# Optimization experiments

Measured on AMD Instinct MI355X. Metric: run time of the kernel, lower is better.

The kernel has to match this reference:

```python
import jax, jax.numpy as jnp
import numpy as np

D_MODEL = 1024
NHEAD = 16
NUM_KV = 4
D_K = D_MODEL // NHEAD          # 64
GROUP = NHEAD // NUM_KV          # 4 query heads per kv head
ROPE_BASE = 10000.0


def _rope(x, seq_len):
    """Apply rotary embedding. x: [B, h, S, d_k], positions 0..seq_len-1."""
    half = D_K // 2
    inv_freq = 1.0 / (ROPE_BASE ** (jnp.arange(0, D_K, 2, dtype=jnp.float32) / D_K))
    t = jnp.arange(seq_len, dtype=jnp.float32)
    freqs = jnp.outer(t, inv_freq)                      # [S, d_k/2]
    emb = jnp.concatenate([freqs, freqs], axis=-1)      # [S, d_k]
    cos, sin = jnp.cos(emb), jnp.sin(emb)               # broadcast over B, h
    x1, x2 = x[..., :half], x[..., half:]
    rot = jnp.concatenate([-x2, x1], axis=-1)
    return x * cos + rot * sin


def setup_inputs() -> dict:
    key = jax.random.key(0)
    ks = jax.random.split(key, 12)
    B, S = 2, 2048
    s_in = 1.0 / np.sqrt(D_MODEL)
    inp = {
        "query": jax.random.normal(ks[0], (B, S, D_MODEL), jnp.float32),
        "key":   jax.random.normal(ks[1], (B, S, D_MODEL), jnp.float32),
        "value": jax.random.normal(ks[2], (B, S, D_MODEL), jnp.float32),
        "Wq": jax.random.normal(ks[3], (D_MODEL, D_MODEL), jnp.float32) * s_in,
        "bq": jnp.zeros((D_MODEL,), jnp.float32),
        "Wk": jax.random.normal(ks[4], (NUM_KV * D_K, D_MODEL), jnp.float32) * s_in,
        "bk": jnp.zeros((NUM_KV * D_K,), jnp.float32),
        "Wv": jax.random.normal(ks[5], (NUM_KV * D_K, D_MODEL), jnp.float32) * s_in,
        "bv": jnp.zeros((NUM_KV * D_K,), jnp.float32),
        "Wo": jax.random.normal(ks[6], (D_MODEL, D_MODEL), jnp.float32) * s_in,
        "bo": jnp.zeros((D_MODEL,), jnp.float32),
    }
    return inp


def reference(query, key, value, Wq, bq, Wk, bk, Wv, bv, Wo, bo):
    B, S, _ = query.shape
    T = key.shape[1]
    # projections (torch Linear: x @ W^T + b)
    Q = (query @ Wq.T + bq).reshape(B, S, NHEAD, D_K).transpose(0, 2, 1, 3)   # [B,H,S,dk]
    K = (key   @ Wk.T + bk).reshape(B, T, NUM_KV, D_K).transpose(0, 2, 1, 3)  # [B,KV,T,dk]
    V = (value @ Wv.T + bv).reshape(B, T, NUM_KV, D_K).transpose(0, 2, 1, 3)
    # fused RoPE (start_pos = 0)
    Q = _rope(Q, S)
    K = _rope(K, T)
    # expand kv heads (repeat_interleave on head dim)
    Kr = jnp.repeat(K, GROUP, axis=1)   # [B,H,T,dk]
    Vr = jnp.repeat(V, GROUP, axis=1)
    scale = 1.0 / np.sqrt(D_K)
    scores = jnp.einsum("bhsd,bhtd->bhst", Q, Kr) * scale   # [B,H,S,T]
    attn = jax.nn.softmax(scores, axis=-1)                    # dropout = eval/no-op
    context = jnp.einsum("bhst,bhtd->bhsd", attn, Vr)        # [B,H,S,dk]
    context = context.transpose(0, 2, 1, 3).reshape(B, S, D_MODEL)
    return context @ Wo.T + bo
```

## Files before the change

### kernel.cpp

```cpp
#include <hip/hip_runtime.h>
#include <hip/hip_bf16.h>

typedef __hip_bfloat16 bf16;
typedef __attribute__((ext_vector_type(8))) short short8;
typedef __attribute__((ext_vector_type(4))) short short4v;
typedef __attribute__((ext_vector_type(4))) float f32x4;
typedef __attribute__((ext_vector_type(4))) float float4v;

static __device__ inline short f2bf(float f){
  __hip_bfloat16 h = __float2bfloat16(f);
  return *reinterpret_cast<short*>(&h);
}

static __device__ __forceinline__ unsigned cvt_pk_bf16(float lo, float hi){
  unsigned r;
  asm("v_cvt_pk_bf16_f32 %0, %1, %2" : "=v"(r) : "v"(lo), "v"(hi));
  return r;
}

static __device__ __forceinline__ float exp2_fast(float x){
  float r;
  asm("v_exp_f32 %0, %1" : "=v"(r) : "v"(x));
  return r;
}

static __device__ __forceinline__ float max3f(float a, float b, float c){
  float r;
  asm("v_max3_f32 %0, %1, %2, %3" : "=v"(r) : "v"(a), "v"(b), "v"(c));
  return r;
}

static __device__ inline short8 load8(const float* p){
  float4v a = *reinterpret_cast<const float4v*>(p);
  float4v b = *reinterpret_cast<const float4v*>(p + 4);
  short8 r;
  unsigned* u = reinterpret_cast<unsigned*>(&r);
  u[0] = cvt_pk_bf16(a[0], a[1]);
  u[1] = cvt_pk_bf16(a[2], a[3]);
  u[2] = cvt_pk_bf16(b[0], b[1]);
  u[3] = cvt_pk_bf16(b[2], b[3]);
  return r;
}
static __device__ inline short8 load8(const bf16* p){
  return *reinterpret_cast<const short8*>(p);
}

typedef __attribute__((address_space(1))) const unsigned int gas_u32;
typedef __attribute__((address_space(3))) unsigned int las_u32;
static __device__ __forceinline__ void gload16(const void* g, void* l){
  __builtin_amdgcn_global_load_lds((gas_u32*)g, (las_u32*)l, 16, 0, 0);
}

template<int N>
static __device__ __forceinline__ void vm_barrier(){
  if constexpr (N == 8) asm volatile("s_waitcnt vmcnt(8)" ::: "memory");
  else if constexpr (N == 4) asm volatile("s_waitcnt vmcnt(4)" ::: "memory");
  else if constexpr (N == 2) asm volatile("s_waitcnt vmcnt(2)" ::: "memory");
  else asm volatile("s_waitcnt vmcnt(0)" ::: "memory");
  __builtin_amdgcn_s_barrier();
  __builtin_amdgcn_sched_barrier(0);
}

#define CVT_Q   0
#define CVT_K   4194304
#define CVT_V   8388608
#define CVT_WQ  12582912
#define CVT_WK  13631488
#define CVT_WV  13893632
#define CVT_WO  14155776
#define CVT_TOT 15204352
__global__ void cvt_kernel(bf16* __restrict__ dst, float* __restrict__ tab,
    const float* q, const float* k, const float* v,
    const float* wq, const float* wk, const float* wv, const float* wo){
  if (blockIdx.x < 256){
    const int idx = blockIdx.x * 256 + threadIdx.x;
    const int d = idx & 31, s = idx >> 5;
    const float ang = (float)s * exp2f(-0.41524101186092030f * (float)d);
    float sn, cs;
    sincosf(ang, &sn, &cs);
    tab[idx*2] = cs; tab[idx*2+1] = sn;
  }
  const size_t i8 = ((size_t)blockIdx.x * 256 + threadIdx.x) * 8;
  const float* src; size_t off;
  if      (i8 < CVT_K ){ src = q;  off = i8; }
  else if (i8 < CVT_V ){ src = k;  off = i8 - CVT_K; }
  else if (i8 < CVT_WQ){ src = v;  off = i8 - CVT_V; }
  else if (i8 < CVT_WK){ src = wq; off = i8 - CVT_WQ; }
  else if (i8 < CVT_WV){ src = wk; off = i8 - CVT_WK; }
  else if (i8 < CVT_WO){ src = wv; off = i8 - CVT_WV; }
  else                 { src = wo; off = i8 - CVT_WO; }
  *reinterpret_cast<short8*>(reinterpret_cast<short*>(dst) + i8) = load8(src + off);
}

template<int MODE>
__device__ __forceinline__ void gemm_bt_v2(
    short* lds, void* __restrict__ Cout,
    const bf16* __restrict__ A, const bf16* __restrict__ B,
    const float* __restrict__ bias, const float* __restrict__ tab,
    int ntile, int N, int K)
{
  const int NK = K >> 5;
  const int n0 = ntile * 128, m0 = blockIdx.y * 128;
  const int tid = threadIdx.x, w = tid >> 6, lane = tid & 63;
  const int wm = w >> 1, wn = w & 1, lr = lane & 15, lg = lane >> 4;
  const int r0 = w*32 + (lane >> 2), r1 = r0 + 16;
  const int c0 = ((lane & 3) ^ ((r0 >> 1) & 3)) * 8;
  const int c1 = ((lane & 3) ^ ((r1 >> 1) & 3)) * 8;
  const bf16* A0 = A + (size_t)(m0 + r0) * K + c0;
  const bf16* A1 = A + (size_t)(m0 + r1) * K + c1;
  const bf16* B0 = B + (size_t)(n0 + r0) * K + c0;
  const bf16* B1 = B + (size_t)(n0 + r1) * K + c1;
  const int ldsW = (w*32) * 32;
  int offA[4], offB[4];
  #pragma unroll
  for (int i = 0; i < 4; i++){
    const int ra = wm*64 + i*16 + lr;
    offA[i] = ra*64 + ((lg ^ ((ra >> 1) & 3)) * 16);
    const int rb = wn*64 + i*16 + lr;
    offB[i] = rb*64 + ((lg ^ ((rb >> 1) & 3)) * 16);
  }
  auto stage = [&](int t){
    short* bufA = lds + (t & 3) * 8192;
    short* bufB = bufA + 4096;
    gload16(A0 + t*32, bufA + ldsW);
    gload16(A1 + t*32, bufA + ldsW + 512);
    gload16(B0 + t*32, bufB + ldsW);
    gload16(B1 + t*32, bufB + ldsW + 512);
  };
  f32x4 acc[4][4] = {};
  stage(0); stage(1);
  for (int t = 0; t < NK; t++){
    if (t + 2 < NK){ stage(t + 2); vm_barrier<8>(); }
    else if (t + 1 < NK){ vm_barrier<4>(); }
    else { vm_barrier<0>(); }
    const char* bufA = (const char*)(lds + (t & 3) * 8192);
    const char* bufB = bufA + 8192;
    short8 af[4], bfm[4];
    #pragma unroll
    for (int mt = 0; mt < 4; mt++) af[mt]  = *(const short8*)(bufA + offA[mt]);
    #pragma unroll
    for (int nt = 0; nt < 4; nt++) bfm[nt] = *(const short8*)(bufB + offB[nt]);
    __builtin_amdgcn_s_setprio(1);
    #pragma unroll
    for (int mt = 0; mt < 4; mt++)
      #pragma unroll
      for (int nt = 0; nt < 4; nt++)
        acc[mt][nt] = __builtin_amdgcn_mfma_f32_16x16x32_bf16(af[mt], bfm[nt], acc[mt][nt], 0, 0, 0);
    __builtin_amdgcn_s_setprio(0);
  }
  if constexpr (MODE == 0){
    float* C = (float*)Cout;
    #pragma unroll
    for (int mt = 0; mt < 4; mt++){
      #pragma unroll
      for (int nt = 0; nt < 4; nt++){
        const int col = n0 + wn*64 + nt*16 + lr;
        const float bv = bias[col];
        const int rbase = m0 + wm*64 + mt*16 + lg*4;
        #pragma unroll
        for (int i = 0; i < 4; i++)
          C[(size_t)(rbase + i) * N + col] = acc[mt][nt][i] + bv;
      }
    }
  } else if constexpr (MODE == 1 || MODE == 2){
    bf16* dst = (bf16*)Cout;
    constexpr int NH = (MODE == 1) ? 16 : 4;
    constexpr float SC = (MODE == 1) ? 0.18033688011112042f : 1.0f;
    #pragma unroll
    for (int mt = 0; mt < 4; mt++){
      #pragma unroll
      for (int nt = 0; nt < 2; nt++){
        const int col = n0 + wn*64 + nt*16 + lr;
        const int d = col & 63;
        const int hh = col >> 6;
        const float b1 = bias[col], b2 = bias[col + 32];
        #pragma unroll
        for (int i = 0; i < 4; i++){
          const int m = m0 + wm*64 + mt*16 + lg*4 + i;
          const int s = m & 2047, bb = m >> 11;
          const float cs = tab[(s*32 + d)*2], sn = tab[(s*32 + d)*2 + 1];
          const float x1 = acc[mt][nt][i] + b1;
          const float x2 = acc[mt][nt+2][i] + b2;
          const size_t o = ((size_t)(bb*NH + hh) * 2048 + s) * 64 + d;
          dst[o]      = __float2bfloat16((x1*cs - x2*sn) * SC);
          dst[o + 32] = __float2bfloat16((x2*cs + x1*sn) * SC);
        }
      }
    }
  } else {
    bf16* dst = (bf16*)Cout;
    #pragma unroll
    for (int mt = 0; mt < 4; mt++){
      #pragma unroll
      for (int nt = 0; nt < 4; nt++){
        const int col = n0 + wn*64 + nt*16 + lr;
        const int kv = col >> 6, d = col & 63;
        const float bv = bias[col];
        #pragma unroll
        for (int i = 0; i < 4; i++){
          const int m = m0 + wm*64 + mt*16 + lg*4 + i;
          const int s = m & 2047, bb = m >> 11;
          dst[((size_t)(bb*4 + kv) * 64 + d) * 2048 + s] = __float2bfloat16(acc[mt][nt][i] + bv);
        }
      }
    }
  }
}

__global__ __launch_bounds__(256, 2) void gemm_qkv_kernel(
    bf16* Qa, bf16* Ka, bf16* Va, const bf16* cvt,
    const float* bq, const float* bk, const float* bv, const float* tab){
  __shared__ short lds[4 * 8192];
  const int x = blockIdx.x;
  if (x < 8)
    gemm_bt_v2<1>(lds, Qa, cvt + CVT_Q, cvt + CVT_WQ, bq, tab, x,    1024, 1024);
  else if (x < 10)
    gemm_bt_v2<2>(lds, Ka, cvt + CVT_K, cvt + CVT_WK, bk, tab, x-8,  256, 1024);
  else
    gemm_bt_v2<3>(lds, Va, cvt + CVT_V, cvt + CVT_WV, bv, tab, x-10, 256, 1024);
}
__global__ __launch_bounds__(256, 2) void gemm_out_kernel(
    float* C, const bf16* ctx, const bf16* cvt, const float* bo){
  __shared__ short lds[4 * 8192];
  gemm_bt_v2<0>(lds, C, ctx, cvt + CVT_WO, bo, nullptr, blockIdx.x, 1024, 1024);
}

__global__ __launch_bounds__(256, 2) void attn_kernel(
    bf16* __restrict__ ctx, const bf16* __restrict__ Qa,
    const bf16* __restrict__ Ka, const bf16* __restrict__ Vt)
{
  __shared__ short Klds[4][64 * 64];
  __shared__ short Vlds[4][64 * 64];
  const int bh = blockIdx.y, b = bh >> 4, h = bh & 15, kvh = h >> 2;
  const int q0 = blockIdx.x * 128;
  const int tid = threadIdx.x, w = tid >> 6, lane = tid & 63;
  const int lr = lane & 15, lg = lane >> 4;
  const bf16* Qbase = Qa + (size_t)bh * 2048 * 64;
  const bf16* Kbase = Ka + (size_t)(b*4 + kvh) * 2048 * 64;
  const bf16* Vbase = Vt + (size_t)(b*4 + kvh) * 64 * 2048;

  short8 qf[2][2];
  #pragma unroll
  for (int qt = 0; qt < 2; qt++){
    qf[qt][0] = load8(Qbase + (size_t)(q0 + w*32 + qt*16 + lr) * 64 + lg*8);
    qf[qt][1] = load8(Qbase + (size_t)(q0 + w*32 + qt*16 + lr) * 64 + 32 + lg*8);
  }

  const int xsw = (lr & 7) << 4;
  const int koff0 = lr*128 + ((lg*16) ^ xsw);
  const int koff1 = lr*128 + ((64 + lg*16) ^ xsw);
  int voff[2][2];
  #pragma unroll
  for (int kkA = 0; kkA < 2; kkA++)
    #pragma unroll
    for (int hh = 0; hh < 2; hh++)
      voff[kkA][hh] = lr*128 + ((kkA*64 + lg*8 + hh*32) ^ xsw);

  const int l8 = lane >> 3;
  const int ch = (lane & 7) ^ l8;
  const bf16* kSrc = Kbase + (size_t)(w*16 + l8) * 64 + ch*8;
  const bf16* vSrc = Vbase + (size_t)(w*16 + l8) * 2048 + ch*8;
  auto stage = [&](int bi, int t){
    short* Kd = &Klds[bi][(w*16) * 64];
    short* Vd = &Vlds[bi][(w*16) * 64];
    const bf16* ks = kSrc + (size_t)t * 64 * 64;
    const bf16* vs = vSrc + t * 64;
    gload16(ks,           Kd);
    gload16(ks + 8*64,    Kd + 8*64);
    gload16(vs,           Vd);
    gload16(vs + 8*2048,  Vd + 8*64);
  };

  float mrow[2] = {-1e30f, -1e30f};
  f32x4 o[2][4] = {};
  f32x4 acc_l[2] = {};
  short8 ones;
  #pragma unroll
  for (int j = 0; j < 4; j++) reinterpret_cast<unsigned*>(&ones)[j] = 0x3F803F80u;

  auto qk = [&](const char* Kc, f32x4 (&st)[4][2]){
    __builtin_amdgcn_s_setprio(1);
    #pragma unroll
    for (int mt = 0; mt < 4; mt++){
      short8 kf0 = *reinterpret_cast<const short8*>(Kc + mt*2048 + koff0);
      short8 kf1 = *reinterpret_cast<const short8*>(Kc + mt*2048 + koff1);
      #pragma unroll
      for (int qt = 0; qt < 2; qt++){
        st[mt][qt] = __builtin_amdgcn_mfma_f32_16x16x32_bf16(kf0, qf[qt][0], (f32x4){0.f,0.f,0.f,0.f}, 0, 0, 0);
        st[mt][qt] = __builtin_amdgcn_mfma_f32_16x16x32_bf16(kf1, qf[qt][1], st[mt][qt], 0, 0, 0);
      }
    }
    __builtin_amdgcn_s_setprio(0);
  };

  auto softmax_pv = [&](f32x4 (&st)[4][2], const char* Vc){
    short8 pf[2][2];
    #pragma unroll
    for (int qt = 0; qt < 2; qt++){
      const float m0 = max3f(st[0][qt][0], st[0][qt][1], st[0][qt][2]);
      const float m1 = max3f(st[0][qt][3], st[1][qt][0], st[1][qt][1]);
      const float m2 = max3f(st[1][qt][2], st[1][qt][3], st[2][qt][0]);
      const float m3 = max3f(st[2][qt][1], st[2][qt][2], st[2][qt][3]);
      const float m4 = max3f(st[3][qt][0], st[3][qt][1], st[3][qt][2]);
      float mx = fmaxf(max3f(m0, m1, m2), max3f(m3, m4, st[3][qt][3]));
      if (__any(mx > mrow[qt] + 8.0f)){
        mx = fmaxf(mx, __shfl_xor(mx, 16));
        mx = fmaxf(mx, __shfl_xor(mx, 32));
        const float nm = fmaxf(mrow[qt], mx);
        const float alpha = exp2_fast(mrow[qt] - nm);
        mrow[qt] = nm;
        float ab[4];
        #pragma unroll
        for (int i = 0; i < 4; i++) ab[i] = __shfl(alpha, lg*4 + i);
        #pragma unroll
        for (int dt = 0; dt < 4; dt++)
          #pragma unroll
          for (int i = 0; i < 4; i++)
            o[qt][dt][i] *= ab[i];
        #pragma unroll
        for (int i = 0; i < 4; i++) acc_l[qt][i] *= ab[i];
      }
      unsigned* pw = reinterpret_cast<unsigned*>(&pf[qt][0]);
      #pragma unroll
      for (int j = 0; j < 8; j++){
        const int mt = j >> 1, i0 = (j & 1) * 2;
        const float e0 = exp2_fast(st[mt][qt][i0]     - mrow[qt]);
        const float e1 = exp2_fast(st[mt][qt][i0 + 1] - mrow[qt]);
        pw[j] = cvt_pk_bf16(e0, e1);
      }
    }
    __builtin_amdgcn_s_setprio(1);
    #pragma unroll
    for (int qt = 0; qt < 2; qt++){
      acc_l[qt] = __builtin_amdgcn_mfma_f32_16x16x32_bf16(pf[qt][0], ones, acc_l[qt], 0, 0, 0);
      acc_l[qt] = __builtin_amdgcn_mfma_f32_16x16x32_bf16(pf[qt][1], ones, acc_l[qt], 0, 0, 0);
    }
    #pragma unroll
    for (int dt = 0; dt < 4; dt++){
      #pragma unroll
      for (int kkA = 0; kkA < 2; kkA++){
        short8 vf;
        *reinterpret_cast<short4v*>(&vf) =
            *reinterpret_cast<const short4v*>(Vc + dt*2048 + voff[kkA][0]);
        *reinterpret_cast<short4v*>(reinterpret_cast<short*>(&vf) + 4) =
            *reinterpret_cast<const short4v*>(Vc + dt*2048 + voff[kkA][1]);
        #pragma unroll
        for (int qt = 0; qt < 2; qt++)
          o[qt][dt] = __builtin_amdgcn_mfma_f32_16x16x32_bf16(pf[qt][kkA], vf, o[qt][dt], 0, 0, 0);
      }
    }
    __builtin_amdgcn_s_setprio(0);
  };

  f32x4 stA[4][2], stB[4][2];

  stage(0, 0); stage(1, 1);
  vm_barrier<4>();
  qk((const char*)&Klds[0][0], stA);

  for (int tt = 0; tt < 32; tt += 2){
    if (tt + 2 < 32){ stage((tt+2) & 3, tt+2); vm_barrier<4>(); }
    else vm_barrier<0>();
    qk((const char*)&Klds[(tt+1) & 3][0], stB);
    softmax_pv(stA, (const char*)&Vlds[tt & 3][0]);
    if (tt + 3 < 32){ stage((tt+3) & 3, tt+3); vm_barrier<4>(); }
    else vm_barrier<0>();
    if (tt + 2 < 32) qk((const char*)&Klds[(tt+2) & 3][0], stA);
    softmax_pv(stB, (const char*)&Vlds[(tt+1) & 3][0]);
  }

  #pragma unroll
  for (int qt = 0; qt < 2; qt++){
    float lb[4];
    #pragma unroll
    for (int i = 0; i < 4; i++) lb[i] = 1.0f / acc_l[qt][i];
    #pragma unroll
    for (int dt = 0; dt < 4; dt++){
      #pragma unroll
      for (int i = 0; i < 4; i++){
        const int q = q0 + w*32 + qt*16 + lg*4 + i;
        ctx[(size_t)(b*2048 + q) * 1024 + h*64 + dt*16 + lr] =
            __float2bfloat16(o[qt][dt][i] * lb[i]);
      }
    }
  }
}

extern "C" void kernel_launch(void* const* d_in, const int* in_sizes, int n_in,
                              void* d_out, int out_size, void* d_ws, size_t ws_size,
                              hipStream_t stream)
{
  const float* query = (const float*)d_in[0];
  const float* key   = (const float*)d_in[1];
  const float* value = (const float*)d_in[2];
  const float* Wq = (const float*)d_in[3];
  const float* bq = (const float*)d_in[4];
  const float* Wk = (const float*)d_in[5];
  const float* bk = (const float*)d_in[6];
  const float* Wv = (const float*)d_in[7];
  const float* bv = (const float*)d_in[8];
  const float* Wo = (const float*)d_in[9];
  const float* bo = (const float*)d_in[10];
  float* out = (float*)d_out;

  char* ws = (char*)d_ws;
  size_t off = 0;
  float* tab = (float*)(ws + off); off += (size_t)2048 * 32 * 2 * 4;
  bf16*  Qa  = (bf16*)(ws + off);  off += (size_t)32 * 2048 * 64 * 2;
  bf16*  Ka  = (bf16*)(ws + off);  off += (size_t)8 * 2048 * 64 * 2;
  bf16*  Va  = (bf16*)(ws + off);  off += (size_t)8 * 64 * 2048 * 2;
  bf16*  ctx = (bf16*)(ws + off);  off += (size_t)2 * 2048 * 1024 * 2;
  bf16*  cvt = (bf16*)(ws + off);  off += (size_t)CVT_TOT * 2;

  cvt_kernel<<<CVT_TOT / 8 / 256, 256, 0, stream>>>(cvt, tab, query, key, value, Wq, Wk, Wv, Wo);
  gemm_qkv_kernel<<<dim3(12, 32), 256, 0, stream>>>(Qa, Ka, Va, cvt, bq, bk, bv, tab);
  attn_kernel<<<dim3(16, 32), 256, 0, stream>>>(ctx, Qa, Ka, Va);
  gemm_out_kernel<<<dim3(8, 32), 256, 0, stream>>>(out, ctx, cvt, bo);
}
```

Baseline: 106.5 us.

## Fuse fp32 activation conversion into QKV GEMM and remap attention block order

The QKV projection GEMM now loads fp32 activations straight into LDS through a three-buffer pipeline and converts them to bf16 in registers before the MFMAs. The conversion kernel therefore only handles the weights. This is meant to remove the large activation round-trip through a bf16 workspace. The attention grid index is also remapped so that concurrently running blocks share KV heads, to improve cache reuse. In exchange, the GEMM loads twice as many bytes per A tile and spends extra ALU on conversions.

```diff
diff --git a/kernel.cpp b/kernel.cpp
--- a/kernel.cpp
+++ b/kernel.cpp
@@ -54,23 +54,19 @@
 template<int N>
 static __device__ __forceinline__ void vm_barrier(){
   if constexpr (N == 8) asm volatile("s_waitcnt vmcnt(8)" ::: "memory");
+  else if constexpr (N == 6) asm volatile("s_waitcnt vmcnt(6)" ::: "memory");
   else if constexpr (N == 4) asm volatile("s_waitcnt vmcnt(4)" ::: "memory");
-  else if constexpr (N == 2) asm volatile("s_waitcnt vmcnt(2)" ::: "memory");
   else asm volatile("s_waitcnt vmcnt(0)" ::: "memory");
   __builtin_amdgcn_s_barrier();
   __builtin_amdgcn_sched_barrier(0);
 }
 
-#define CVT_Q   0
-#define CVT_K   4194304
-#define CVT_V   8388608
-#define CVT_WQ  12582912
-#define CVT_WK  13631488
-#define CVT_WV  13893632
-#define CVT_WO  14155776
-#define CVT_TOT 15204352
+#define CW_WQ  0
+#define CW_WK  1048576
+#define CW_WV  1310720
+#define CW_WO  1572864
+#define CW_TOT 2621440
 __global__ void cvt_kernel(bf16* __restrict__ dst, float* __restrict__ tab,
-    const float* q, const float* k, const float* v,
     const float* wq, const float* wk, const float* wv, const float* wo){
   if (blockIdx.x < 256){
     const int idx = blockIdx.x * 256 + threadIdx.x;
@@ -82,22 +78,144 @@
   }
   const size_t i8 = ((size_t)blockIdx.x * 256 + threadIdx.x) * 8;
   const float* src; size_t off;
-  if      (i8 < CVT_K ){ src = q;  off = i8; }
-  else if (i8 < CVT_V ){ src = k;  off = i8 - CVT_K; }
-  else if (i8 < CVT_WQ){ src = v;  off = i8 - CVT_V; }
-  else if (i8 < CVT_WK){ src = wq; off = i8 - CVT_WQ; }
-  else if (i8 < CVT_WV){ src = wk; off = i8 - CVT_WK; }
-  else if (i8 < CVT_WO){ src = wv; off = i8 - CVT_WV; }
-  else                 { src = wo; off = i8 - CVT_WO; }
+  if      (i8 < CW_WK){ src = wq; off = i8; }
+  else if (i8 < CW_WV){ src = wk; off = i8 - CW_WK; }
+  else if (i8 < CW_WO){ src = wv; off = i8 - CW_WV; }
+  else                { src = wo; off = i8 - CW_WO; }
   *reinterpret_cast<short8*>(reinterpret_cast<short*>(dst) + i8) = load8(src + off);
 }
 
 template<int MODE>
-__device__ __forceinline__ void gemm_bt_v2(
-    short* lds, void* __restrict__ Cout,
-    const bf16* __restrict__ A, const bf16* __restrict__ B,
+__device__ __forceinline__ void gemm_f32a(
+    char* lds, void* __restrict__ Cout,
+    const float* __restrict__ A, const bf16* __restrict__ B,
     const float* __restrict__ bias, const float* __restrict__ tab,
     int ntile, int N, int K)
+{
+  const int NK = K >> 5;
+  const int n0 = ntile * 128, m0 = blockIdx.y * 128;
+  const int tid = threadIdx.x, w = tid >> 6, lane = tid & 63;
+  const int wm = w >> 1, wn = w & 1, lr = lane & 15, lg = lane >> 4;
+  const int l8 = lane >> 3, gA = lane & 7;
+  const float* Asrc[4];
+  #pragma unroll
+  for (int j = 0; j < 4; j++)
+    Asrc[j] = A + (size_t)(m0 + w*32 + j*8 + l8) * K + ((gA ^ l8) * 4);
+  const int s4 = lane >> 2, gB = lane & 3;
+  const bf16* Bsrc[2];
+  #pragma unroll
+  for (int j = 0; j < 2; j++)
+    Bsrc[j] = B + (size_t)(n0 + w*32 + j*16 + s4) * K + ((gB ^ ((s4 >> 1) & 3)) * 8);
+  const int swA = lr & 7, swB = (lr >> 1) & 3;
+  int offAlo[4], offAhi[4], offB[4];
+  #pragma unroll
+  for (int i = 0; i < 4; i++){
+    const int ra = wm*64 + i*16 + lr;
+    offAlo[i] = ra*128 + ((2*lg)     ^ swA) * 16;
+    offAhi[i] = ra*128 + ((2*lg + 1) ^ swA) * 16;
+    const int rb = wn*64 + i*16 + lr;
+    offB[i]   = rb*64  + ((lg ^ swB) * 16);
+  }
+  auto stage = [&](char* buf, int t){
+    char* dA = buf + w*4096;
+    char* dB = buf + 16384 + w*2048;
+    #pragma unroll
+    for (int j = 0; j < 4; j++) gload16(Asrc[j] + t*32, dA + j*1024);
+    #pragma unroll
+    for (int j = 0; j < 2; j++) gload16(Bsrc[j] + t*32, dB + j*1024);
+  };
+  char* b0 = lds;
+  char* b1 = lds + 24576;
+  char* b2 = lds + 49152;
+  f32x4 acc[4][4] = {};
+  stage(b0, 0); stage(b1, 1);
+  for (int t = 0; t < NK; t++){
+    if (t < NK-1) vm_barrier<6>(); else vm_barrier<0>();
+    if (t + 2 < NK) stage(b2, t + 2);
+    short8 af[4], bfm[4];
+    #pragma unroll
+    for (int i = 0; i < 4; i++){
+      float4v lo = *reinterpret_cast<const float4v*>(b0 + offAlo[i]);
+      float4v hi = *reinterpret_cast<const float4v*>(b0 + offAhi[i]);
+      unsigned* u = reinterpret_cast<unsigned*>(&af[i]);
+      u[0] = cvt_pk_bf16(lo[0], lo[1]); u[1] = cvt_pk_bf16(lo[2], lo[3]);
+      u[2] = cvt_pk_bf16(hi[0], hi[1]); u[3] = cvt_pk_bf16(hi[2], hi[3]);
+    }
+    #pragma unroll
+    for (int i = 0; i < 4; i++)
+      bfm[i] = *reinterpret_cast<const short8*>(b0 + 16384 + offB[i]);
+    __builtin_amdgcn_s_setprio(1);
+    #pragma unroll
+    for (int mt = 0; mt < 4; mt++)
+      #pragma unroll
+      for (int nt = 0; nt < 4; nt++)
+        acc[mt][nt] = __builtin_amdgcn_mfma_f32_16x16x32_bf16(af[mt], bfm[nt], acc[mt][nt], 0, 0, 0);
+    __builtin_amdgcn_s_setprio(0);
+    char* tmp = b0; b0 = b1; b1 = b2; b2 = tmp;
+  }
+  if constexpr (MODE == 1 || MODE == 2){
+    bf16* dst = (bf16*)Cout;
+    constexpr int NH = (MODE == 1) ? 16 : 4;
+    constexpr float SC = (MODE == 1) ? 0.18033688011112042f : 1.0f;
+    #pragma unroll
+    for (int mt = 0; mt < 4; mt++){
+      #pragma unroll
+      for (int nt = 0; nt < 2; nt++){
+        const int col = n0 + wn*64 + nt*16 + lr;
+        const int d = col & 63;
+        const int hh = col >> 6;
+        const float b1v = bias[col], b2v = bias[col + 32];
+        #pragma unroll
+        for (int i = 0; i < 4; i++){
+          const int m = m0 + wm*64 + mt*16 + lg*4 + i;
+          const int s = m & 2047, bb = m >> 11;
+          const float cs = tab[(s*32 + d)*2], sn = tab[(s*32 + d)*2 + 1];
+          const float x1 = acc[mt][nt][i] + b1v;
+          const float x2 = acc[mt][nt+2][i] + b2v;
+          const size_t o = ((size_t)(bb*NH + hh) * 2048 + s) * 64 + d;
+          dst[o]      = __float2bfloat16((x1*cs - x2*sn) * SC);
+          dst[o + 32] = __float2bfloat16((x2*cs + x1*sn) * SC);
+        }
+      }
+    }
+  } else {
+    bf16* dst = (bf16*)Cout;
+    #pragma unroll
+    for (int mt = 0; mt < 4; mt++){
+      #pragma unroll
+      for (int nt = 0; nt < 4; nt++){
+        const int col = n0 + wn*64 + nt*16 + lr;
+        const int kv = col >> 6, d = col & 63;
+        const float bv = bias[col];
+        #pragma unroll
+        for (int i = 0; i < 4; i++){
+          const int m = m0 + wm*64 + mt*16 + lg*4 + i;
+          const int s = m & 2047, bb = m >> 11;
+          dst[((size_t)(bb*4 + kv) * 64 + d) * 2048 + s] = __float2bfloat16(acc[mt][nt][i] + bv);
+        }
+      }
+    }
+  }
+}
+
+__global__ __launch_bounds__(256, 2) void gemm_qkv_kernel(
+    bf16* Qa, bf16* Ka, bf16* Va,
+    const float* query, const float* key, const float* value, const bf16* cw,
+    const float* bq, const float* bk, const float* bv, const float* tab){
+  __shared__ char lds[3 * 24576];
+  const int x = blockIdx.x;
+  if (x < 8)
+    gemm_f32a<1>(lds, Qa, query, cw + CW_WQ, bq, tab, x,    1024, 1024);
+  else if (x < 10)
+    gemm_f32a<2>(lds, Ka, key,   cw + CW_WK, bk, tab, x-8,  256, 1024);
+  else
+    gemm_f32a<3>(lds, Va, value, cw + CW_WV, bv, tab, x-10, 256, 1024);
+}
+
+__device__ __forceinline__ void gemm_bt_out(
+    short* lds, float* __restrict__ C,
+    const bf16* __restrict__ A, const bf16* __restrict__ B,
+    const float* __restrict__ bias, int ntile, int N, int K)
 {
   const int NK = K >> 5;
   const int n0 = ntile * 128, m0 = blockIdx.y * 128;
@@ -148,81 +266,24 @@
         acc[mt][nt] = __builtin_amdgcn_mfma_f32_16x16x32_bf16(af[mt], bfm[nt], acc[mt][nt], 0, 0, 0);
     __builtin_amdgcn_s_setprio(0);
   }
-  if constexpr (MODE == 0){
-    float* C = (float*)Cout;
-    #pragma unroll
-    for (int mt = 0; mt < 4; mt++){
-      #pragma unroll
-      for (int nt = 0; nt < 4; nt++){
-        const int col = n0 + wn*64 + nt*16 + lr;
-        const float bv = bias[col];
-        const int rbase = m0 + wm*64 + mt*16 + lg*4;
-        #pragma unroll
-        for (int i = 0; i < 4; i++)
-          C[(size_t)(rbase + i) * N + col] = acc[mt][nt][i] + bv;
-      }
-    }
-  } else if constexpr (MODE == 1 || MODE == 2){
-    bf16* dst = (bf16*)Cout;
-    constexpr int NH = (MODE == 1) ? 16 : 4;
-    constexpr float SC = (MODE == 1) ? 0.18033688011112042f : 1.0f;
-    #pragma unroll
-    for (int mt = 0; mt < 4; mt++){
-      #pragma unroll
-      for (int nt = 0; nt < 2; nt++){
-        const int col = n0 + wn*64 + nt*16 + lr;
-        const int d = col & 63;
-        const int hh = col >> 6;
-        const float b1 = bias[col], b2 = bias[col + 32];
-        #pragma unroll
-        for (int i = 0; i < 4; i++){
-          const int m = m0 + wm*64 + mt*16 + lg*4 + i;
-          const int s = m & 2047, bb = m >> 11;
-          const float cs = tab[(s*32 + d)*2], sn = tab[(s*32 + d)*2 + 1];
-          const float x1 = acc[mt][nt][i] + b1;
-          const float x2 = acc[mt][nt+2][i] + b2;
-          const size_t o = ((size_t)(bb*NH + hh) * 2048 + s) * 64 + d;
-          dst[o]      = __float2bfloat16((x1*cs - x2*sn) * SC);
-          dst[o + 32] = __float2bfloat16((x2*cs + x1*sn) * SC);
-        }
-      }
-    }
-  } else {
-    bf16* dst = (bf16*)Cout;
-    #pragma unroll
-    for (int mt = 0; mt < 4; mt++){
-      #pragma unroll
-      for (int nt = 0; nt < 4; nt++){
-        const int col = n0 + wn*64 + nt*16 + lr;
-        const int kv = col >> 6, d = col & 63;
-        const float bv = bias[col];
-        #pragma unroll
-        for (int i = 0; i < 4; i++){
-          const int m = m0 + wm*64 + mt*16 + lg*4 + i;
-          const int s = m & 2047, bb = m >> 11;
-          dst[((size_t)(bb*4 + kv) * 64 + d) * 2048 + s] = __float2bfloat16(acc[mt][nt][i] + bv);
-        }
-      }
-    }
-  }
-}
-
-__global__ __launch_bounds__(256, 2) void gemm_qkv_kernel(
-    bf16* Qa, bf16* Ka, bf16* Va, const bf16* cvt,
-    const float* bq, const float* bk, const float* bv, const float* tab){
+  #pragma unroll
+  for (int mt = 0; mt < 4; mt++){
+    #pragma unroll
+    for (int nt = 0; nt < 4; nt++){
+      const int col = n0 + wn*64 + nt*16 + lr;
+      const float bv = bias[col];
+      const int rbase = m0 + wm*64 + mt*16 + lg*4;
+      #pragma unroll
+      for (int i = 0; i < 4; i++)
+        C[(size_t)(rbase + i) * N + col] = acc[mt][nt][i] + bv;
+    }
+  }
+}
+
+__global__ __launch_bounds__(256, 2) void gemm_out_kernel(
+    float* C, const bf16* ctx, const bf16* cw, const float* bo){
   __shared__ short lds[4 * 8192];
-  const int x = blockIdx.x;
-  if (x < 8)
-    gemm_bt_v2<1>(lds, Qa, cvt + CVT_Q, cvt + CVT_WQ, bq, tab, x,    1024, 1024);
-  else if (x < 10)
-    gemm_bt_v2<2>(lds, Ka, cvt + CVT_K, cvt + CVT_WK, bk, tab, x-8,  256, 1024);
-  else
-    gemm_bt_v2<3>(lds, Va, cvt + CVT_V, cvt + CVT_WV, bv, tab, x-10, 256, 1024);
-}
-__global__ __launch_bounds__(256, 2) void gemm_out_kernel(
-    float* C, const bf16* ctx, const bf16* cvt, const float* bo){
-  __shared__ short lds[4 * 8192];
-  gemm_bt_v2<0>(lds, C, ctx, cvt + CVT_WO, bo, nullptr, blockIdx.x, 1024, 1024);
+  gemm_bt_out(lds, C, ctx, cw + CW_WO, bo, blockIdx.x, 1024, 1024);
 }
 
 __global__ __launch_bounds__(256, 2) void attn_kernel(
@@ -231,8 +292,10 @@
 {
   __shared__ short Klds[4][64 * 64];
   __shared__ short Vlds[4][64 * 64];
-  const int bh = blockIdx.y, b = bh >> 4, h = bh & 15, kvh = h >> 2;
-  const int q0 = blockIdx.x * 128;
+  const int pid = blockIdx.y * 16 + blockIdx.x;
+  const int bh = (pid & 7) * 4 + ((pid >> 3) & 3);
+  const int q0 = (pid >> 5) * 128;
+  const int b = bh >> 4, h = bh & 15, kvh = h >> 2;
   const int tid = threadIdx.x, w = tid >> 6, lane = tid & 63;
   const int lr = lane & 15, lg = lane >> 4;
   const bf16* Qbase = Qa + (size_t)bh * 2048 * 64;
@@ -410,10 +473,11 @@
   bf16*  Ka  = (bf16*)(ws + off);  off += (size_t)8 * 2048 * 64 * 2;
   bf16*  Va  = (bf16*)(ws + off);  off += (size_t)8 * 64 * 2048 * 2;
   bf16*  ctx = (bf16*)(ws + off);  off += (size_t)2 * 2048 * 1024 * 2;
-  bf16*  cvt = (bf16*)(ws + off);  off += (size_t)CVT_TOT * 2;
-
-  cvt_kernel<<<CVT_TOT / 8 / 256, 256, 0, stream>>>(cvt, tab, query, key, value, Wq, Wk, Wv, Wo);
-  gemm_qkv_kernel<<<dim3(12, 32), 256, 0, stream>>>(Qa, Ka, Va, cvt, bq, bk, bv, tab);
+  bf16*  cw  = (bf16*)(ws + off);  off += (size_t)CW_TOT * 2;
+
+  cvt_kernel<<<CW_TOT / 8 / 256, 256, 0, stream>>>(cw, tab, Wq, Wk, Wv, Wo);
+  gemm_qkv_kernel<<<dim3(12, 32), 256, 0, stream>>>(Qa, Ka, Va, query, key, value,
+                                                    cw, bq, bk, bv, tab);
   attn_kernel<<<dim3(16, 32), 256, 0, stream>>>(ctx, Qa, Ka, Va);
-  gemm_out_kernel<<<dim3(8, 32), 256, 0, stream>>>(out, ctx, cvt, bo);
-}
+  gemm_out_kernel<<<dim3(8, 32), 256, 0, stream>>>(out, ctx, cw, bo);
+}
```

Result: slower. 109.5 us (+2.8%).
